# Kernel optimization log

Measured on AMD Instinct MI355X. Metric: run time of the kernel, lower is better.

The kernel has to match this reference:

```python
import jax, jax.numpy as jnp
import numpy as np

B, C, H, W = 2, 256, 128, 128
O = 256          # out_channels
KH = KW = 3
K = KH * KW      # 9 kernel taps
PAD, DIL = 1, 1


def setup_inputs() -> dict:
    key = jax.random.key(0)
    k1, k2, k3, k4, k5 = jax.random.split(key, 5)
    x = jax.random.normal(k1, (B, C, H, W), dtype=jnp.float32)
    # offset/mask predicting conv: 3*groups*K = 27 output channels.
    # scaled small so predicted offsets are O(1) pixels (torch inits these to 0).
    w_off = jax.random.normal(k2, (3 * K, C, KH, KW), dtype=jnp.float32) * 0.01
    b_off = jax.random.normal(k3, (3 * K,), dtype=jnp.float32) * 0.01
    # main weight is 1x1, later tiled to 3x3 (weight.repeat([1,1,3,3]))
    stdv = 1.0 / np.sqrt(C * KH * KW)
    weight = jax.random.uniform(k4, (O, C, 1, 1), dtype=jnp.float32, minval=-stdv, maxval=stdv)
    bias = jax.random.normal(k5, (O,), dtype=jnp.float32) * 0.01
    return {"x": x, "w_off": w_off, "b_off": b_off, "weight": weight, "bias": bias}


def _bilinear_gather(img, py, px):
    # img: [C,H,W]; py/px: [K,H,W] float sample coords. Zero outside bounds.
    y0 = jnp.floor(py).astype(jnp.int32)
    x0 = jnp.floor(px).astype(jnp.int32)
    ly = py - y0
    lx = px - x0

    def corner(yc, xc):
        valid = (yc >= 0) & (yc < H) & (xc >= 0) & (xc < W)
        v = img[:, jnp.clip(yc, 0, H - 1), jnp.clip(xc, 0, W - 1)]  # [C,K,H,W]
        return jnp.where(valid[None], v, 0.0)

    return (corner(y0, x0) * ((1 - ly) * (1 - lx))[None]
            + corner(y0, x0 + 1) * ((1 - ly) * lx)[None]
            + corner(y0 + 1, x0) * (ly * (1 - lx))[None]
            + corner(y0 + 1, x0 + 1) * (ly * lx)[None])


def reference(x, w_off, b_off, weight, bias):
    # --- offset/mask prediction conv (3x3, pad 1) ---
    tmp = jax.lax.conv_general_dilated(
        x, w_off, window_strides=(1, 1), padding=((PAD, PAD), (PAD, PAD)),
        rhs_dilation=(DIL, DIL), dimension_numbers=("NCHW", "OIHW", "NCHW"))
    tmp = tmp + b_off[None, :, None, None]
    o1, o2, mask = tmp[:, :K], tmp[:, K:2 * K], tmp[:, 2 * K:]
    offset = jnp.concatenate([o1, o2], axis=1)          # [B, 2K, H, W]
    dy = offset[:, 0::2]                                # [B, K, H, W]
    dx = offset[:, 1::2]
    # softmax over the SPATIAL axis per mask channel (as in the source)
    mask = jax.nn.softmax(mask.reshape(B, K, H * W), axis=2).reshape(B, K, H, W)

    # --- sampling grid ---
    kk = jnp.arange(K)
    ki = (kk // KW).astype(jnp.float32)
    kj = (kk % KW).astype(jnp.float32)
    base_y = ki[:, None, None] * DIL - PAD + jnp.arange(H, dtype=jnp.float32)[None, :, None]
    base_x = kj[:, None, None] * DIL - PAD + jnp.arange(W, dtype=jnp.float32)[None, None, :]
    py = dy + base_y[None]                              # [B, K, H, W]
    px = dx + base_x[None]

    sampled = jax.vmap(_bilinear_gather)(x, py, px)     # [B, C, K, H, W]
    sampled = sampled * mask[:, None]                   # modulated

    # weight.repeat([1,1,3,3]) -> same 1x1 weight at every tap
    Wk = jnp.tile(weight, (1, 1, KH, KW)).reshape(O, C, K)
    out = jnp.einsum("bckhw,ock->bohw", sampled, Wk) + bias[None, :, None, None]
    return out
```

## Files before the change

### kernel.cpp

```cpp
#include <hip/hip_runtime.h>
#include <hip/hip_fp16.h>

#define Bx 2
#define Cx 256
#define Hx 128
#define Wx 128
#define HWx (Hx*Wx)
#define Ox 256
#define Kx 9
#define NOFF 27
#define KK 2304

#define SLOT 80
#define NSLOT 102
#define ABUF (NSLOT*SLOT)

typedef __attribute__((ext_vector_type(8))) _Float16 f16x8;
typedef __attribute__((ext_vector_type(4))) float f32x4;


__device__ __forceinline__ unsigned short f2h(float f) {
    return __half_as_ushort(__float2half_rn(f));
}

__global__ __launch_bounds__(256) void k_pt(
        const float* __restrict__ x, const float* __restrict__ w_off,
        const float* __restrict__ weight,
        unsigned short* __restrict__ xtb, unsigned short* __restrict__ wb,
        unsigned short* __restrict__ wq) {
    if (blockIdx.x >= 2048) {
        int i = (blockIdx.x - 2048) * 256 + threadIdx.x;
        if (i < 32 * KK) {
            int oc = i / KK;
            int k  = i - oc * KK;
            int tap = k >> 8;
            int c   = k & 255;
            float v = (oc < NOFF) ? w_off[(oc * Cx + c) * 9 + tap] : 0.f;
            wb[i] = f2h(v);
        } else {
            int j = i - 32 * KK;
            if (j < Ox * Cx) wq[j] = f2h(weight[j]);
        }
        return;
    }
    __shared__ float tl[64][65];
    int tid = threadIdx.x;
    int t   = blockIdx.x;
    int b   = t >> 10;
    int r2  = t & 1023;
    int hw0 = (r2 >> 2) * 64;
    int c0  = (r2 & 3) * 64;
#pragma unroll
    for (int r = 0; r < 4; r++) {
        int cl = r * 16 + (tid >> 4);
        int hl = (tid & 15) * 4;
        const float4 v = *(const float4*)&x[((size_t)(b * Cx + c0 + cl)) * HWx + hw0 + hl];
        tl[cl][hl + 0] = v.x; tl[cl][hl + 1] = v.y; tl[cl][hl + 2] = v.z; tl[cl][hl + 3] = v.w;
    }
    __syncthreads();
#pragma unroll
    for (int r = 0; r < 4; r++) {
        int hl = r * 16 + (tid >> 4);
        int cl = (tid & 15) * 4;
        ushort4 o;
        o.x = f2h(tl[cl + 0][hl]); o.y = f2h(tl[cl + 1][hl]);
        o.z = f2h(tl[cl + 2][hl]); o.w = f2h(tl[cl + 3][hl]);
        *(ushort4*)&xtb[((size_t)b * HWx + hw0 + hl) * Cx + c0 + cl] = o;
    }
}

__global__ __launch_bounds__(256) void k1_mfma(
        const unsigned short* __restrict__ xtb, const unsigned short* __restrict__ wb,
        const float* __restrict__ b_off, float* __restrict__ tmp_t,
        float* __restrict__ pscr) {
    int band = blockIdx.x & 7;
    int idx  = blockIdx.x >> 3;
    int y    = band * 16 + (idx >> 2);
    int qt   = idx & 3;
    int px0  = qt * 32;
    int b    = blockIdx.y;

    __shared__ unsigned short As[2 * ABUF];
    __shared__ float wmx[2][9], wsum[2][9];
    int tid  = threadIdx.x;
    int wave = tid >> 6, lane = tid & 63;
    int quad = lane >> 4, col = lane & 15;
    int wmh  = wave >> 1;
    int wn   = wave & 1;

    const unsigned short* xb = xtb + (size_t)b * HWx * Cx;
    const unsigned short* sp[4];
    int  sdst[4];
    bool sstp[4], sldp[4];
#pragma unroll
    for (int i = 0; i < 4; i++) {
        int u = tid + i * 256;
        bool uv = (u < 816);
        int slot = u >> 3;
        int ci   = (u & 7) * 8;
        int r = (slot >= 68) ? 2 : (slot >= 34 ? 1 : 0);
        int p = slot - r * 34;
        int yy = y + r - 1;
        int px = px0 + p - 1;
        bool ib = uv && (yy >= 0) && (yy < Hx) && (px >= 0) && (px < Wx);
        int lin = ib ? (yy * Wx + px) : 0;
        sp[i]   = xb + (size_t)lin * Cx + ci;
        sdst[i] = slot * SLOT + ci;
        sstp[i] = uv;
        sldp[i] = ib;
    }

    f32x4 acc = {};
    const unsigned short* wrow = wb + (size_t)(wn * 16 + col) * KK;
    int abase = (wmh * 16 + col) * SLOT + quad * 8;

    {
        uint4 sreg[4];
#pragma unroll
        for (int i = 0; i < 4; i++)
            sreg[i] = sldp[i] ? *(const uint4*)(sp[i]) : make_uint4(0u, 0u, 0u, 0u);
#pragma unroll
        for (int i = 0; i < 4; i++)
            if (sstp[i]) *(uint4*)&As[sdst[i]] = sreg[i];
    }
    __syncthreads();

#pragma unroll 1
    for (int ph = 0; ph < 4; ph++) {
        const unsigned short* Ab = As + (ph & 1) * ABUF;
        unsigned short*       Aw = As + ((ph & 1) ^ 1) * ABUF;
        uint4 sreg[4];
        if (ph < 3) {
#pragma unroll
            for (int i = 0; i < 4; i++)
                sreg[i] = sldp[i] ? *(const uint4*)(sp[i] + (ph + 1) * 64)
                                  : make_uint4(0u, 0u, 0u, 0u);
        }
#pragma unroll
        for (int s = 0; s < 2; s++) {
            f16x8 breg[9];
#pragma unroll
            for (int t = 0; t < 9; t++)
                breg[t] = *(const f16x8*)(wrow + t * 256 + ph * 64 + s * 32 + quad * 8);
#pragma unroll
            for (int r = 0; r < 3; r++)
#pragma unroll
            for (int dc = 0; dc < 3; dc++) {
                f16x8 a0 = *(const f16x8*)&Ab[(r * 34 + dc) * SLOT + abase + s * 32];
                acc = __builtin_amdgcn_mfma_f32_16x16x32_f16(a0, breg[r * 3 + dc], acc, 0, 0, 0);
            }
        }
        if (ph < 3) {
#pragma unroll
            for (int i = 0; i < 4; i++)
                if (sstp[i]) *(uint4*)&Aw[sdst[i]] = sreg[i];
        }
        __syncthreads();
    }

    float* orow = tmp_t + ((size_t)(b * HWx) + (size_t)y * Wx + px0) * 32;
    int oc = wn * 16 + col;
    float bo = (oc < NOFF) ? b_off[oc] : 0.f;
#pragma unroll
    for (int r4 = 0; r4 < 4; r4++) {
        int pxd = wmh * 16 + quad * 4 + r4;
        float v = acc[r4] + bo;
        acc[r4] = v;
        orow[(size_t)pxd * 32 + oc] = v;
    }

    float m4 = fmaxf(fmaxf(acc[0], acc[1]), fmaxf(acc[2], acc[3]));
    m4 = fmaxf(m4, __shfl_xor(m4, 16));
    m4 = fmaxf(m4, __shfl_xor(m4, 32));
    float s4 = __expf(acc[0] - m4) + __expf(acc[1] - m4)
             + __expf(acc[2] - m4) + __expf(acc[3] - m4);
    s4 += __shfl_xor(s4, 16);
    s4 += __shfl_xor(s4, 32);
    if (wn == 1 && quad == 0 && col >= 2 && col <= 10) {
        wmx[wmh][col - 2] = m4;
        wsum[wmh][col - 2] = s4;
    }
    __syncthreads();
    if (tid < 9) {
        float M = fmaxf(wmx[0][tid], wmx[1][tid]);
        float S = wsum[0][tid] * __expf(wmx[0][tid] - M)
                + wsum[1][tid] * __expf(wmx[1][tid] - M);
        int blkid = y * 4 + qt;
        int pidx  = (b * 9 + tid) * 512 + blkid;
        pscr[pidx] = M;
        pscr[9216 + pidx] = S;
    }
}

__global__ __launch_bounds__(256) void k35_fused(
        const unsigned short* __restrict__ xtb, const float* __restrict__ tmp_t,
        const float* __restrict__ pscr, const unsigned short* __restrict__ wq,
        const float* __restrict__ bias, float* __restrict__ out) {
    __shared__ __half2 lwh[64][36];
    __shared__ int     lo[64][36];
    __shared__ unsigned short As[64][264];
    __shared__ float sst9[9][2];
    __shared__ float xm[4][9], xe[4][9];
    int tid  = threadIdx.x;
    int band = blockIdx.x & 7;
    int sub  = blockIdx.x >> 3;
    int b    = blockIdx.y;
    int px0  = (band * 32 + sub) * 64;

    {
        int wv = tid >> 6, ln = tid & 63;
        int s0 = tid * 2;
#pragma unroll 1
        for (int g = 0; g < 9; g++) {
            const float* pm = pscr + (size_t)(b * 9 + g) * 512;
            float m0 = pm[s0], m1 = pm[s0 + 1];
            float e0 = pm[9216 + s0], e1 = pm[9216 + s0 + 1];
            float M = fmaxf(m0, m1);
            float E = e0 * __expf(m0 - M) + e1 * __expf(m1 - M);
            for (int off = 32; off > 0; off >>= 1) {
                float Mo = __shfl_xor(M, off);
                float Eo = __shfl_xor(E, off);
                float Mn = fmaxf(M, Mo);
                E = E * __expf(M - Mn) + Eo * __expf(Mo - Mn);
                M = Mn;
            }
            if (ln == 0) { xm[wv][g] = M; xe[wv][g] = E; }
        }
    }
    __syncthreads();
    if (tid < 9) {
        float Mf = fmaxf(fmaxf(xm[0][tid], xm[1][tid]), fmaxf(xm[2][tid], xm[3][tid]));
        float S = xe[0][tid] * __expf(xm[0][tid] - Mf)
                + xe[1][tid] * __expf(xm[1][tid] - Mf)
                + xe[2][tid] * __expf(xm[2][tid] - Mf)
                + xe[3][tid] * __expf(xm[3][tid] - Mf);
        sst9[tid][0] = Mf;
        sst9[tid][1] = 1.f / S;
    }
    __syncthreads();

    for (int u = tid; u < 576; u += 256) {
        int px = u / 9, k = u - px * 9;
        int hw = px0 + px;
        int y  = hw >> 7;
        int xx = hw & (Wx - 1);
        const float* trow = tmp_t + ((size_t)b * HWx + hw) * 32;
        float dy = trow[2 * k];
        float dx = trow[2 * k + 1];
        float lg = trow[18 + k];
        float m  = __expf(lg - sst9[k][0]) * sst9[k][1] * 256.f;
        float py = dy + (float)(k / 3 - 1 + y);
        float px_ = dx + (float)(k % 3 - 1 + xx);
        float fy = floorf(py), fx = floorf(px_);
        int y0 = (int)fy, x0 = (int)fx;
        float ly = py - fy, lx = px_ - fx;
        float w00 = (1.f - ly) * (1.f - lx) * m;
        float w01 = (1.f - ly) * lx * m;
        float w10 = ly * (1.f - lx) * m;
        float w11 = ly * lx * m;
        int y1 = y0 + 1, x1 = x0 + 1;
        bool vy0 = (y0 >= 0) & (y0 < Hx), vy1 = (y1 >= 0) & (y1 < Hx);
        bool vx0 = (x0 >= 0) & (x0 < Wx), vx1 = (x1 >= 0) & (x1 < Wx);
        int cy0 = min(max(y0, 0), Hx - 1), cy1 = min(max(y1, 0), Hx - 1);
        int cx0 = min(max(x0, 0), Wx - 1), cx1 = min(max(x1, 0), Wx - 1);
        float a00 = (vy0 && vx0) ? w00 : 0.f;
        float a01 = (vy0 && vx1) ? w01 : 0.f;
        float a10 = (vy1 && vx0) ? w10 : 0.f;
        float a11 = (vy1 && vx1) ? w11 : 0.f;
        lwh[px][4 * k + 0] = __half2half2(__float2half_rn(a00));  lo[px][4 * k + 0] = cy0 * Wx + cx0;
        lwh[px][4 * k + 1] = __half2half2(__float2half_rn(a01));  lo[px][4 * k + 1] = cy0 * Wx + cx1;
        lwh[px][4 * k + 2] = __half2half2(__float2half_rn(a10));  lo[px][4 * k + 2] = cy1 * Wx + cx0;
        lwh[px][4 * k + 3] = __half2half2(__float2half_rn(a11));  lo[px][4 * k + 3] = cy1 * Wx + cx1;
    }
    __syncthreads();

    int wave = tid >> 6;
    int lane = tid & 63;
    int half = lane >> 5;
    int li   = lane & 31;
    const unsigned short* xb = xtb + (size_t)b * HWx * Cx + li * 8;
    const __half2 uns = __half2half2(__float2half_rn(1.f / 256.f));
#pragma unroll 1
    for (int pass = 0; pass < 8; pass++) {
        int px = wave * 16 + pass * 2 + half;
        __half2 a0 = __half2half2(__ushort_as_half(0));
        __half2 a1 = a0, a2 = a0, a3 = a0;
#pragma unroll
        for (int j = 0; j < 36; j++) {
            __half2 w = lwh[px][j];
            int   off = lo[px][j];
            uint4 v = *(const uint4*)(xb + (size_t)off * Cx);
            a0 = __hfma2(w, *(__half2*)&v.x, a0);
            a1 = __hfma2(w, *(__half2*)&v.y, a1);
            a2 = __hfma2(w, *(__half2*)&v.z, a2);
            a3 = __hfma2(w, *(__half2*)&v.w, a3);
        }
        a0 = __hmul2(a0, uns); a1 = __hmul2(a1, uns);
        a2 = __hmul2(a2, uns); a3 = __hmul2(a3, uns);
        uint4 r;
        r.x = *(unsigned*)&a0; r.y = *(unsigned*)&a1;
        r.z = *(unsigned*)&a2; r.w = *(unsigned*)&a3;
        *(uint4*)&As[px][li * 8] = r;
    }
    __syncthreads();

    int quad = lane >> 4, col = lane & 15;
    f32x4 acc[4][4] = {};
#pragma unroll
    for (int ki = 0; ki < 8; ki++) {
        int k0 = ki * 32;
        f16x8 a[4], w[4];
#pragma unroll
        for (int mt = 0; mt < 4; mt++)
            a[mt] = *(const f16x8*)&As[mt * 16 + col][k0 + quad * 8];
#pragma unroll
        for (int nt = 0; nt < 4; nt++)
            w[nt] = *(const f16x8*)(wq + (size_t)(wave * 64 + nt * 16 + col) * Cx + k0 + quad * 8);
#pragma unroll
        for (int mt = 0; mt < 4; mt++)
#pragma unroll
            for (int nt = 0; nt < 4; nt++)
                acc[mt][nt] = __builtin_amdgcn_mfma_f32_16x16x32_f16(a[mt], w[nt], acc[mt][nt], 0, 0, 0);
    }

#pragma unroll
    for (int nt = 0; nt < 4; nt++) {
        int oc = wave * 64 + nt * 16 + col;
        float bo = bias[oc];
#pragma unroll
        for (int mt = 0; mt < 4; mt++) {
            int hw = px0 + mt * 16 + quad * 4;
            float4 v;
            v.x = acc[mt][nt][0] + bo; v.y = acc[mt][nt][1] + bo;
            v.z = acc[mt][nt][2] + bo; v.w = acc[mt][nt][3] + bo;
            *(float4*)&out[((size_t)(b * Ox + oc)) * HWx + hw] = v;
        }
    }
}

extern "C" void kernel_launch(void* const* d_in, const int* in_sizes, int n_in,
                              void* d_out, int out_size, void* d_ws, size_t ws_size,
                              hipStream_t stream) {
    const float*    x      = (const float*)d_in[0];
    const float*    w_off  = (const float*)d_in[1];
    const float*    b_off  = (const float*)d_in[2];
    const float*    weight = (const float*)d_in[3];
    const float*    bias   = (const float*)d_in[4];
    float* out = (float*)d_out;
    float* ws  = (float*)d_ws;

    float*          tmp_t = ws;
    unsigned short* wbq   = (unsigned short*)(ws + 1048640);
    unsigned short* xtb   = (unsigned short*)(ws + 1085504);
    unsigned short* wq    = (unsigned short*)(ws + 5279808);
    float*          pscr  = ws + 5312576;

    k_pt<<<dim3(2592), 256, 0, stream>>>(x, w_off, weight, xtb, wbq, wq);
    k1_mfma<<<dim3(512, Bx), 256, 0, stream>>>(xtb, wbq, b_off, tmp_t, pscr);
    k35_fused<<<dim3(256, Bx), 256, 0, stream>>>(xtb, tmp_t, pscr, wq, bias, out);
}
```

Baseline: 166.4 us.

## Replace two-pass softmax max/sum partials with atomic exp-sum, halve fused tile

```diff
diff --git a/kernel.cpp b/kernel.cpp
--- a/kernel.cpp
+++ b/kernel.cpp
@@ -27,8 +27,9 @@
         const float* __restrict__ x, const float* __restrict__ w_off,
         const float* __restrict__ weight,
         unsigned short* __restrict__ xtb, unsigned short* __restrict__ wb,
-        unsigned short* __restrict__ wq) {
+        unsigned short* __restrict__ wq, float* __restrict__ stats) {
     if (blockIdx.x >= 2048) {
+        if (blockIdx.x == 2048 && threadIdx.x < 32) stats[threadIdx.x] = 0.f;
         int i = (blockIdx.x - 2048) * 256 + threadIdx.x;
         if (i < 32 * KK) {
             int oc = i / KK;
@@ -69,10 +70,10 @@
     }
 }
 
-__global__ __launch_bounds__(256) void k1_mfma(
+__global__ __launch_bounds__(256, 4) void k1_mfma(
         const unsigned short* __restrict__ xtb, const unsigned short* __restrict__ wb,
         const float* __restrict__ b_off, float* __restrict__ tmp_t,
-        float* __restrict__ pscr) {
+        float* __restrict__ stats) {
     int band = blockIdx.x & 7;
     int idx  = blockIdx.x >> 3;
     int y    = band * 16 + (idx >> 2);
@@ -81,7 +82,7 @@
     int b    = blockIdx.y;
 
     __shared__ unsigned short As[2 * ABUF];
-    __shared__ float wmx[2][9], wsum[2][9];
+    __shared__ float wsum[2][9];
     int tid  = threadIdx.x;
     int wave = tid >> 6, lane = tid & 63;
     int quad = lane >> 4, col = lane & 15;
@@ -169,77 +170,34 @@
         orow[(size_t)pxd * 32 + oc] = v;
     }
 
-    float m4 = fmaxf(fmaxf(acc[0], acc[1]), fmaxf(acc[2], acc[3]));
-    m4 = fmaxf(m4, __shfl_xor(m4, 16));
-    m4 = fmaxf(m4, __shfl_xor(m4, 32));
-    float s4 = __expf(acc[0] - m4) + __expf(acc[1] - m4)
-             + __expf(acc[2] - m4) + __expf(acc[3] - m4);
+    float s4 = __expf(acc[0]) + __expf(acc[1]) + __expf(acc[2]) + __expf(acc[3]);
     s4 += __shfl_xor(s4, 16);
     s4 += __shfl_xor(s4, 32);
-    if (wn == 1 && quad == 0 && col >= 2 && col <= 10) {
-        wmx[wmh][col - 2] = m4;
+    if (wn == 1 && quad == 0 && col >= 2 && col <= 10)
         wsum[wmh][col - 2] = s4;
-    }
-    __syncthreads();
-    if (tid < 9) {
-        float M = fmaxf(wmx[0][tid], wmx[1][tid]);
-        float S = wsum[0][tid] * __expf(wmx[0][tid] - M)
-                + wsum[1][tid] * __expf(wmx[1][tid] - M);
-        int blkid = y * 4 + qt;
-        int pidx  = (b * 9 + tid) * 512 + blkid;
-        pscr[pidx] = M;
-        pscr[9216 + pidx] = S;
-    }
-}
-
-__global__ __launch_bounds__(256) void k35_fused(
+    __syncthreads();
+    if (tid < 9)
+        atomicAdd(&stats[b * 9 + tid], wsum[0][tid] + wsum[1][tid]);
+}
+
+__global__ __launch_bounds__(256, 4) void k35_fused(
         const unsigned short* __restrict__ xtb, const float* __restrict__ tmp_t,
-        const float* __restrict__ pscr, const unsigned short* __restrict__ wq,
+        const float* __restrict__ stats, const unsigned short* __restrict__ wq,
         const float* __restrict__ bias, float* __restrict__ out) {
-    __shared__ __half2 lwh[64][36];
-    __shared__ int     lo[64][36];
-    __shared__ unsigned short As[64][264];
-    __shared__ float sst9[9][2];
-    __shared__ float xm[4][9], xe[4][9];
+    __shared__ __half2 lwh[32][36];
+    __shared__ int     lo[32][36];
+    __shared__ unsigned short As[32][264];
+    __shared__ float sst9[9];
     int tid  = threadIdx.x;
     int band = blockIdx.x & 7;
     int sub  = blockIdx.x >> 3;
     int b    = blockIdx.y;
-    int px0  = (band * 32 + sub) * 64;
-
-    {
-        int wv = tid >> 6, ln = tid & 63;
-        int s0 = tid * 2;
-#pragma unroll 1
-        for (int g = 0; g < 9; g++) {
-            const float* pm = pscr + (size_t)(b * 9 + g) * 512;
-            float m0 = pm[s0], m1 = pm[s0 + 1];
-            float e0 = pm[9216 + s0], e1 = pm[9216 + s0 + 1];
-            float M = fmaxf(m0, m1);
-            float E = e0 * __expf(m0 - M) + e1 * __expf(m1 - M);
-            for (int off = 32; off > 0; off >>= 1) {
-                float Mo = __shfl_xor(M, off);
-                float Eo = __shfl_xor(E, off);
-                float Mn = fmaxf(M, Mo);
-                E = E * __expf(M - Mn) + Eo * __expf(Mo - Mn);
-                M = Mn;
-            }
-            if (ln == 0) { xm[wv][g] = M; xe[wv][g] = E; }
-        }
-    }
-    __syncthreads();
-    if (tid < 9) {
-        float Mf = fmaxf(fmaxf(xm[0][tid], xm[1][tid]), fmaxf(xm[2][tid], xm[3][tid]));
-        float S = xe[0][tid] * __expf(xm[0][tid] - Mf)
-                + xe[1][tid] * __expf(xm[1][tid] - Mf)
-                + xe[2][tid] * __expf(xm[2][tid] - Mf)
-                + xe[3][tid] * __expf(xm[3][tid] - Mf);
-        sst9[tid][0] = Mf;
-        sst9[tid][1] = 1.f / S;
-    }
-    __syncthreads();
-
-    for (int u = tid; u < 576; u += 256) {
+    int px0  = (band * 64 + sub) * 32;
+
+    if (tid < 9) sst9[tid] = 256.f / stats[b * Kx + tid];
+    __syncthreads();
+
+    for (int u = tid; u < 288; u += 256) {
         int px = u / 9, k = u - px * 9;
         int hw = px0 + px;
         int y  = hw >> 7;
@@ -248,7 +206,7 @@
         float dy = trow[2 * k];
         float dx = trow[2 * k + 1];
         float lg = trow[18 + k];
-        float m  = __expf(lg - sst9[k][0]) * sst9[k][1] * 256.f;
+        float m  = __expf(lg) * sst9[k];
         float py = dy + (float)(k / 3 - 1 + y);
         float px_ = dx + (float)(k % 3 - 1 + xx);
         float fy = floorf(py), fx = floorf(px_);
@@ -281,8 +239,8 @@
     const unsigned short* xb = xtb + (size_t)b * HWx * Cx + li * 8;
     const __half2 uns = __half2half2(__float2half_rn(1.f / 256.f));
 #pragma unroll 1
-    for (int pass = 0; pass < 8; pass++) {
-        int px = wave * 16 + pass * 2 + half;
+    for (int pass = 0; pass < 4; pass++) {
+        int px = wave * 8 + pass * 2 + half;
         __half2 a0 = __half2half2(__ushort_as_half(0));
         __half2 a1 = a0, a2 = a0, a3 = a0;
 #pragma unroll
@@ -305,19 +263,19 @@
     __syncthreads();
 
     int quad = lane >> 4, col = lane & 15;
-    f32x4 acc[4][4] = {};
+    f32x4 acc[2][4] = {};
 #pragma unroll
     for (int ki = 0; ki < 8; ki++) {
         int k0 = ki * 32;
-        f16x8 a[4], w[4];
-#pragma unroll
-        for (int mt = 0; mt < 4; mt++)
+        f16x8 a[2], w[4];
+#pragma unroll
+        for (int mt = 0; mt < 2; mt++)
             a[mt] = *(const f16x8*)&As[mt * 16 + col][k0 + quad * 8];
 #pragma unroll
         for (int nt = 0; nt < 4; nt++)
             w[nt] = *(const f16x8*)(wq + (size_t)(wave * 64 + nt * 16 + col) * Cx + k0 + quad * 8);
 #pragma unroll
-        for (int mt = 0; mt < 4; mt++)
+        for (int mt = 0; mt < 2; mt++)
 #pragma unroll
             for (int nt = 0; nt < 4; nt++)
                 acc[mt][nt] = __builtin_amdgcn_mfma_f32_16x16x32_f16(a[mt], w[nt], acc[mt][nt], 0, 0, 0);
@@ -328,7 +286,7 @@
         int oc = wave * 64 + nt * 16 + col;
         float bo = bias[oc];
 #pragma unroll
-        for (int mt = 0; mt < 4; mt++) {
+        for (int mt = 0; mt < 2; mt++) {
             int hw = px0 + mt * 16 + quad * 4;
             float4 v;
             v.x = acc[mt][nt][0] + bo; v.y = acc[mt][nt][1] + bo;
@@ -353,9 +311,9 @@
     unsigned short* wbq   = (unsigned short*)(ws + 1048640);
     unsigned short* xtb   = (unsigned short*)(ws + 1085504);
     unsigned short* wq    = (unsigned short*)(ws + 5279808);
-    float*          pscr  = ws + 5312576;
-
-    k_pt<<<dim3(2592), 256, 0, stream>>>(x, w_off, weight, xtb, wbq, wq);
-    k1_mfma<<<dim3(512, Bx), 256, 0, stream>>>(xtb, wbq, b_off, tmp_t, pscr);
-    k35_fused<<<dim3(256, Bx), 256, 0, stream>>>(xtb, tmp_t, pscr, wq, bias, out);
-}
+    float*          stats = ws + 5312576;
+
+    k_pt<<<dim3(2592), 256, 0, stream>>>(x, w_off, weight, xtb, wbq, wq, stats);
+    k1_mfma<<<dim3(512, Bx), 256, 0, stream>>>(xtb, wbq, b_off, tmp_t, stats);
+    k35_fused<<<dim3(512, Bx), 256, 0, stream>>>(xtb, tmp_t, stats, wq, bias, out);
+}
```

Result: slower. 171.0 us (+2.7%).
